# Performance work log

Measured on AMD Instinct MI355X. Metric: run time of the kernel, lower is better.

## Reference

```python
import jax, jax.numpy as jnp
import numpy as np


def setup_inputs() -> dict:
    key = jax.random.key(0)
    k1, k2, k3 = jax.random.split(key, 3)
    B, C_IN, C_OUT, K, S = 2, 16, 16, 3, 24
    x = jax.random.normal(k1, (B, C_IN, S, S, S, S), dtype=jnp.float32)
    # weight in canonical [out, in, kh, kw, kd, kt] layout (the torch module's
    # pre-permutation is a storage detail; the math is a standard 4D cross-correlation)
    w = jax.random.normal(k2, (C_OUT, C_IN, K, K, K, K), dtype=jnp.float32) * 0.05
    b = jax.random.normal(k3, (C_OUT,), dtype=jnp.float32) * 0.05
    return {"x": x, "w": w, "b": b}


def reference(x, w, b):
    # 4D convolution with 'same' padding (pad = k//2 in every spatial dim),
    # stride 1, no dilation — exactly what the looped conv4d() computes.
    dn = jax.lax.conv_dimension_numbers(x.shape, w.shape, ("NCHWDT", "OIHWDT", "NCHWDT"))
    out = jax.lax.conv_general_dilated(
        x, w,
        window_strides=(1, 1, 1, 1),
        padding="SAME",
        dimension_numbers=dn,
    )
    return out + b[None, :, None, None, None, None]
```

## Files before the change

kernel.cpp:

```cpp
#include <hip/hip_runtime.h>

typedef __attribute__((ext_vector_type(8))) short bfrag;
typedef __attribute__((ext_vector_type(4))) float f32x4;

#define XS4 331776
#define XS3 13824
#define XS2 576

__global__ void wsplit_kernel(const float* __restrict__ w,
                              unsigned int* __restrict__ wfrag) {
    int e = blockIdx.x * 256 + threadIdx.x;
    int ci2 = e & 3;
    int co  = (e >> 2) & 15;
    int t84 = e >> 6;
    int tau = t84 % 84;
    int cs  = t84 / 84;
    int ch  = cs >> 1;
    int s   = cs & 1;

    unsigned int outv = 0u;
    if (tau < 81) {
        unsigned int half[2];
#pragma unroll
        for (int q = 0; q < 2; ++q) {
            int ci = ch * 8 + ci2 * 2 + q;
            union { float f; unsigned u; } v;
            v.f = w[(co * 16 + ci) * 81 + tau];
            unsigned hi = v.u & 0xFFFF0000u;
            union { unsigned u; float f; } hv; hv.u = hi;
            union { float f; unsigned u; } rv; rv.f = v.f - hv.f;
            unsigned lo = rv.u & 0xFFFF0000u;
            half[q] = (s == 0) ? hi : lo;
        }
        outv = (half[0] >> 16) | (half[1] & 0xFFFF0000u);
    }
    wfrag[e] = outv;
}

__global__ __launch_bounds__(192, 3)
void conv4d_mfma(const float* __restrict__ x,
                 const unsigned short* __restrict__ wfrag,
                 const float* __restrict__ bias,
                 float* __restrict__ out) {
    __shared__ __align__(16) unsigned short xhl[2][1260][8];

    const int tid = threadIdx.x;
    const int l   = tid & 63;

    int bid = blockIdx.x;
    const int b    = bid / 3456;
    int r          = bid % 3456;
    const int h    = r / 144;
    r              = r % 144;
    const int w0   = r / 6;
    const int seg  = r % 6;
    const int dseg = seg >> 1;
    const int tseg = seg & 1;
    const int dbase = dseg * 8, tbase = tseg * 12;

    const int i_  = l & 15;
    const int tl4 = l >> 4;
    const int d_i = i_ >> 2;
    const int t_i = i_ & 3;
    const int co  = l & 15;

    const int wv  = tid >> 6;
    const int mt0 = wv * 2, mt1 = wv * 2 + 1;
    const int dq0 = mt0 / 3, tq0 = mt0 % 3;
    const int dq1 = mt1 / 3, tq1 = mt1 % 3;
    const int la0 = dq0 * 896 + tq0 * 64 + d_i * 224 + t_i * 16;
    const int la1 = dq1 * 896 + tq1 * 64 + d_i * 224 + t_i * 16;

    f32x4 acc0 = {0.f, 0.f, 0.f, 0.f};
    f32x4 acc1 = {0.f, 0.f, 0.f, 0.f};

    const char* xbase = (const char*)&xhl[0][0][0];
    const char* wB    = (const char*)wfrag + tl4 * 256 + co * 16;

    for (int ch = 0; ch < 2; ++ch) {
        __syncthreads();

        for (int k = 0; k < 7; ++k) {
            int idx = tid + k * 192;
            if (idx < 1260) {
                int p  = idx / 140;
                int rr = idx - p * 140;
                int dd = rr / 14;
                int tt = rr - dd * 14;
                int hh = h  + p / 3 - 1;
                int ww = w0 + p % 3 - 1;
                int dp = dbase + dd - 1;
                int tp = tbase + tt - 1;
                unsigned hib[8], lob[8];
                bool valid = ((unsigned)hh < 24u) && ((unsigned)ww < 24u) &&
                             ((unsigned)dp < 24u) && ((unsigned)tp < 24u);
                if (valid) {
                    int g = b * (16 * XS4) + (ch * 8) * XS4
                          + hh * XS3 + ww * XS2 + dp * 24 + tp;
#pragma unroll
                    for (int c = 0; c < 8; ++c) {
                        union { float f; unsigned u; } v;
                        v.f = x[g + c * XS4];
                        unsigned hi = v.u & 0xFFFF0000u;
                        union { unsigned u; float f; } hv; hv.u = hi;
                        union { float f; unsigned u; } rv2; rv2.f = v.f - hv.f;
                        hib[c] = hi;
                        lob[c] = rv2.u & 0xFFFF0000u;
                    }
                } else {
#pragma unroll
                    for (int c = 0; c < 8; ++c) { hib[c] = 0u; lob[c] = 0u; }
                }
                uint4 ph, pl;
                ph.x = (hib[0] >> 16) | (hib[1] & 0xFFFF0000u);
                ph.y = (hib[2] >> 16) | (hib[3] & 0xFFFF0000u);
                ph.z = (hib[4] >> 16) | (hib[5] & 0xFFFF0000u);
                ph.w = (hib[6] >> 16) | (hib[7] & 0xFFFF0000u);
                pl.x = (lob[0] >> 16) | (lob[1] & 0xFFFF0000u);
                pl.y = (lob[2] >> 16) | (lob[3] & 0xFFFF0000u);
                pl.z = (lob[4] >> 16) | (lob[5] & 0xFFFF0000u);
                pl.w = (lob[6] >> 16) | (lob[7] & 0xFFFF0000u);
                *(uint4*)((char*)&xhl[0][0][0] + idx * 16)         = ph;
                *(uint4*)((char*)&xhl[0][0][0] + 20160 + idx * 16) = pl;
            }
        }
        __syncthreads();

        const char* pw = wB + ch * 43008;

#pragma unroll
        for (int g = 0; g < 21; ++g) {
            bfrag whf = *(const bfrag*)(pw + g * 1024);
            bfrag wlf = *(const bfrag*)(pw + g * 1024 + 21504);

            int tau  = 4 * g + tl4;
            int teff = tau > 80 ? 80 : tau;
            int p    = teff / 9;
            int r9   = teff - p * 9;
            int kd   = r9 / 3;
            int kt   = r9 - kd * 3;
            int aoff = p * 2240 + kd * 224 + kt * 16;

            const char* ax = xbase + aoff;
            bfrag xh0 = *(const bfrag*)(ax + la0);
            bfrag xl0 = *(const bfrag*)(ax + la0 + 20160);
            bfrag xh1 = *(const bfrag*)(ax + la1);
            bfrag xl1 = *(const bfrag*)(ax + la1 + 20160);

            acc0 = __builtin_amdgcn_mfma_f32_16x16x32_bf16(xh0, whf, acc0, 0, 0, 0);
            acc1 = __builtin_amdgcn_mfma_f32_16x16x32_bf16(xh1, whf, acc1, 0, 0, 0);
            acc0 = __builtin_amdgcn_mfma_f32_16x16x32_bf16(xh0, wlf, acc0, 0, 0, 0);
            acc1 = __builtin_amdgcn_mfma_f32_16x16x32_bf16(xh1, wlf, acc1, 0, 0, 0);
            acc0 = __builtin_amdgcn_mfma_f32_16x16x32_bf16(xl0, whf, acc0, 0, 0, 0);
            acc1 = __builtin_amdgcn_mfma_f32_16x16x32_bf16(xl1, whf, acc1, 0, 0, 0);
        }
    }

    const float bv = bias[co];
    const int ob = (b * 16 + co) * XS4 + h * XS3 + w0 * XS2;
    {
        int d = dbase + dq0 * 4 + tl4;
        int t = tbase + tq0 * 4;
        float4 v;
        v.x = acc0[0] + bv; v.y = acc0[1] + bv;
        v.z = acc0[2] + bv; v.w = acc0[3] + bv;
        *(float4*)&out[ob + d * 24 + t] = v;
    }
    {
        int d = dbase + dq1 * 4 + tl4;
        int t = tbase + tq1 * 4;
        float4 v;
        v.x = acc1[0] + bv; v.y = acc1[1] + bv;
        v.z = acc1[2] + bv; v.w = acc1[3] + bv;
        *(float4*)&out[ob + d * 24 + t] = v;
    }
}

extern "C" void kernel_launch(void* const* d_in, const int* in_sizes, int n_in,
                              void* d_out, int out_size, void* d_ws, size_t ws_size,
                              hipStream_t stream) {
    const float* x    = (const float*)d_in[0];
    const float* w    = (const float*)d_in[1];
    const float* bias = (const float*)d_in[2];
    float* out        = (float*)d_out;
    unsigned int* wsw = (unsigned int*)d_ws;

    wsplit_kernel<<<84, 256, 0, stream>>>(w, wsw);
    conv4d_mfma<<<6912, 192, 0, stream>>>(x, (const unsigned short*)wsw, bias, out);
}
```

Baseline: 243.1 us.

## Pre-split input to bf16 hi/lo in workspace and stage via global_load_lds

Adds a separate pass that splits the fp32 input once into packed bf16 hi/lo halves in workspace. The conv kernel then copies 16-byte records straight into LDS with global_load_lds, using a zero buffer for padded sites. This removes the redundant per-block split of halo data, which covers about 9x the tile, and the strided 8-channel gathers. In exchange it costs an extra full read and write of the input, needs a large workspace with a fallback path, and adds setprio around the MFMA groups plus precomputed LDS offsets.

```diff
diff --git a/kernel.cpp b/kernel.cpp
--- a/kernel.cpp
+++ b/kernel.cpp
@@ -7,8 +7,16 @@
 #define XS3 13824
 #define XS2 576
 
+#define WS_ZERO   86016
+#define WS_XS     86080
+#define XS_HALF_B 5308416
+#define WS_NEED   42553408ull
+#define NSITE     1260
+#define NSITE_PAD 1280
+#define LDS_LO    20480
+
 __global__ void wsplit_kernel(const float* __restrict__ w,
-                              unsigned int* __restrict__ wfrag) {
+                              unsigned int* __restrict__ ws) {
     int e = blockIdx.x * 256 + threadIdx.x;
     int ci2 = e & 3;
     int co  = (e >> 2) & 15;
@@ -34,18 +42,50 @@
         }
         outv = (half[0] >> 16) | (half[1] & 0xFFFF0000u);
     }
-    wfrag[e] = outv;
+    ws[e] = outv;
+    if (e < 16) ws[(WS_ZERO / 4) + e] = 0u;
+}
+
+__global__ void xsplit_kernel(const float* __restrict__ x,
+                              unsigned short* __restrict__ xs) {
+    int s4 = blockIdx.x * 256 + threadIdx.x;
+    int bc = blockIdx.y;
+    const float* xp = x + (size_t)(bc * 8) * XS4 + s4;
+    unsigned hib[8], lob[8];
+#pragma unroll
+    for (int c = 0; c < 8; ++c) {
+        union { float f; unsigned u; } v;
+        v.f = xp[(size_t)c * XS4];
+        unsigned hi = v.u & 0xFFFF0000u;
+        union { unsigned u; float f; } hv; hv.u = hi;
+        union { float f; unsigned u; } rv; rv.f = v.f - hv.f;
+        hib[c] = hi;
+        lob[c] = rv.u & 0xFFFF0000u;
+    }
+    uint4 ph, pl;
+    ph.x = (hib[0] >> 16) | (hib[1] & 0xFFFF0000u);
+    ph.y = (hib[2] >> 16) | (hib[3] & 0xFFFF0000u);
+    ph.z = (hib[4] >> 16) | (hib[5] & 0xFFFF0000u);
+    ph.w = (hib[6] >> 16) | (hib[7] & 0xFFFF0000u);
+    pl.x = (lob[0] >> 16) | (lob[1] & 0xFFFF0000u);
+    pl.y = (lob[2] >> 16) | (lob[3] & 0xFFFF0000u);
+    pl.z = (lob[4] >> 16) | (lob[5] & 0xFFFF0000u);
+    pl.w = (lob[6] >> 16) | (lob[7] & 0xFFFF0000u);
+    *(uint4*)(xs + ((size_t)(bc * 2 + 0) * XS4 + s4) * 8) = ph;
+    *(uint4*)(xs + ((size_t)(bc * 2 + 1) * XS4 + s4) * 8) = pl;
 }
 
 __global__ __launch_bounds__(192, 3)
-void conv4d_mfma(const float* __restrict__ x,
-                 const unsigned short* __restrict__ wfrag,
-                 const float* __restrict__ bias,
-                 float* __restrict__ out) {
-    __shared__ __align__(16) unsigned short xhl[2][1260][8];
-
-    const int tid = threadIdx.x;
-    const int l   = tid & 63;
+void conv4d_mfma_v2(const unsigned short* __restrict__ xs,
+                    const unsigned short* __restrict__ wfrag,
+                    const char* __restrict__ zptr,
+                    const float* __restrict__ bias,
+                    float* __restrict__ out) {
+    __shared__ __align__(16) unsigned short xhl[2 * NSITE_PAD * 8];
+
+    const int tid  = threadIdx.x;
+    const int l    = tid & 63;
+    const int wv   = tid >> 6;
 
     int bid = blockIdx.x;
     const int b    = bid / 3456;
@@ -54,9 +94,140 @@
     r              = r % 144;
     const int w0   = r / 6;
     const int seg  = r % 6;
-    const int dseg = seg >> 1;
-    const int tseg = seg & 1;
-    const int dbase = dseg * 8, tbase = tseg * 12;
+    const int dbase = (seg >> 1) * 8, tbase = (seg & 1) * 12;
+
+    const int i_  = l & 15;
+    const int tl4 = l >> 4;
+    const int d_i = i_ >> 2;
+    const int t_i = i_ & 3;
+    const int co  = l & 15;
+
+    const int mt0 = wv * 2, mt1 = wv * 2 + 1;
+    const int dq0 = mt0 / 3, tq0 = mt0 % 3;
+    const int dq1 = mt1 / 3, tq1 = mt1 % 3;
+    const int la0 = dq0 * 896 + tq0 * 64 + d_i * 224 + t_i * 16;
+    const int la1 = dq1 * 896 + tq1 * 64 + d_i * 224 + t_i * 16;
+
+    int aoffs[21];
+#pragma unroll
+    for (int g = 0; g < 21; ++g) {
+        int tau  = 4 * g + tl4;
+        int teff = tau > 80 ? 80 : tau;
+        int p    = teff / 9;
+        int r9   = teff - p * 9;
+        int kd   = r9 / 3;
+        int kt   = r9 - kd * 3;
+        aoffs[g] = p * 2240 + kd * 224 + kt * 16;
+    }
+
+    f32x4 acc0 = {0.f, 0.f, 0.f, 0.f};
+    f32x4 acc1 = {0.f, 0.f, 0.f, 0.f};
+
+    const char* xbase = (const char*)&xhl[0];
+    const char* xsb   = (const char*)xs;
+    const char* wB    = (const char*)wfrag + tl4 * 256 + co * 16;
+
+    for (int ch = 0; ch < 2; ++ch) {
+        __syncthreads();
+
+        const unsigned base16 = (unsigned)((b * 2 + ch) * 2) * (unsigned)(XS4 * 16);
+
+        for (int k = 0; k < 7; ++k) {
+            int idx0 = k * 192 + wv * 64;
+            if (idx0 < NSITE_PAD) {
+                int idx = idx0 + l;
+                int p  = idx / 140;
+                int rr = idx - p * 140;
+                int dd = rr / 14;
+                int tt = rr - dd * 14;
+                int hh = h  + p / 3 - 1;
+                int ww = w0 + p % 3 - 1;
+                int dp = dbase + dd - 1;
+                int tp = tbase + tt - 1;
+                bool valid = ((unsigned)hh < 24u) && ((unsigned)ww < 24u) &&
+                             ((unsigned)dp < 24u) && ((unsigned)tp < 24u) &&
+                             (idx < NSITE);
+                const char* gh = zptr;
+                const char* gl = zptr;
+                if (valid) {
+                    unsigned off = base16 +
+                        (unsigned)(hh * XS3 + ww * XS2 + dp * 24 + tp) * 16u;
+                    gh = xsb + off;
+                    gl = gh + XS_HALF_B;
+                }
+                char* lp = (char*)&xhl[0] + idx * 16;
+                __builtin_amdgcn_global_load_lds(
+                    (const __attribute__((address_space(1))) void*)gh,
+                    (__attribute__((address_space(3))) void*)lp, 16, 0, 0);
+                __builtin_amdgcn_global_load_lds(
+                    (const __attribute__((address_space(1))) void*)gl,
+                    (__attribute__((address_space(3))) void*)(lp + LDS_LO), 16, 0, 0);
+            }
+        }
+        __syncthreads();
+
+        const char* pw = wB + ch * 43008;
+
+#pragma unroll
+        for (int g = 0; g < 21; ++g) {
+            bfrag whf = *(const bfrag*)(pw + g * 1024);
+            bfrag wlf = *(const bfrag*)(pw + g * 1024 + 21504);
+
+            const char* ax = xbase + aoffs[g];
+            bfrag xh0 = *(const bfrag*)(ax + la0);
+            bfrag xl0 = *(const bfrag*)(ax + la0 + LDS_LO);
+            bfrag xh1 = *(const bfrag*)(ax + la1);
+            bfrag xl1 = *(const bfrag*)(ax + la1 + LDS_LO);
+
+            __builtin_amdgcn_s_setprio(1);
+            acc0 = __builtin_amdgcn_mfma_f32_16x16x32_bf16(xh0, whf, acc0, 0, 0, 0);
+            acc1 = __builtin_amdgcn_mfma_f32_16x16x32_bf16(xh1, whf, acc1, 0, 0, 0);
+            acc0 = __builtin_amdgcn_mfma_f32_16x16x32_bf16(xh0, wlf, acc0, 0, 0, 0);
+            acc1 = __builtin_amdgcn_mfma_f32_16x16x32_bf16(xh1, wlf, acc1, 0, 0, 0);
+            acc0 = __builtin_amdgcn_mfma_f32_16x16x32_bf16(xl0, whf, acc0, 0, 0, 0);
+            acc1 = __builtin_amdgcn_mfma_f32_16x16x32_bf16(xl1, whf, acc1, 0, 0, 0);
+            __builtin_amdgcn_s_setprio(0);
+        }
+    }
+
+    const float bv = bias[co];
+    const int ob = (b * 16 + co) * XS4 + h * XS3 + w0 * XS2;
+    {
+        int d = dbase + dq0 * 4 + tl4;
+        int t = tbase + tq0 * 4;
+        float4 v;
+        v.x = acc0[0] + bv; v.y = acc0[1] + bv;
+        v.z = acc0[2] + bv; v.w = acc0[3] + bv;
+        *(float4*)&out[ob + d * 24 + t] = v;
+    }
+    {
+        int d = dbase + dq1 * 4 + tl4;
+        int t = tbase + tq1 * 4;
+        float4 v;
+        v.x = acc1[0] + bv; v.y = acc1[1] + bv;
+        v.z = acc1[2] + bv; v.w = acc1[3] + bv;
+        *(float4*)&out[ob + d * 24 + t] = v;
+    }
+}
+
+__global__ __launch_bounds__(192, 3)
+void conv4d_mfma_v1(const float* __restrict__ x,
+                    const unsigned short* __restrict__ wfrag,
+                    const float* __restrict__ bias,
+                    float* __restrict__ out) {
+    __shared__ __align__(16) unsigned short xhl[2][1260][8];
+
+    const int tid = threadIdx.x;
+    const int l   = tid & 63;
+
+    int bid = blockIdx.x;
+    const int b    = bid / 3456;
+    int r          = bid % 3456;
+    const int h    = r / 144;
+    r              = r % 144;
+    const int w0   = r / 6;
+    const int seg  = r % 6;
+    const int dbase = (seg >> 1) * 8, tbase = (seg & 1) * 12;
 
     const int i_  = l & 15;
     const int tl4 = l >> 4;
@@ -79,7 +250,6 @@
 
     for (int ch = 0; ch < 2; ++ch) {
         __syncthreads();
-
         for (int k = 0; k < 7; ++k) {
             int idx = tid + k * 192;
             if (idx < 1260) {
@@ -127,7 +297,6 @@
         __syncthreads();
 
         const char* pw = wB + ch * 43008;
-
 #pragma unroll
         for (int g = 0; g < 21; ++g) {
             bfrag whf = *(const bfrag*)(pw + g * 1024);
@@ -183,8 +352,18 @@
     const float* w    = (const float*)d_in[1];
     const float* bias = (const float*)d_in[2];
     float* out        = (float*)d_out;
-    unsigned int* wsw = (unsigned int*)d_ws;
-
-    wsplit_kernel<<<84, 256, 0, stream>>>(w, wsw);
-    conv4d_mfma<<<6912, 192, 0, stream>>>(x, (const unsigned short*)wsw, bias, out);
-}
+    char* ws          = (char*)d_ws;
+    unsigned* wfrag   = (unsigned*)ws;
+
+    wsplit_kernel<<<84, 256, 0, stream>>>(w, wfrag);
+
+    if (ws_size >= WS_NEED) {
+        unsigned short* xs = (unsigned short*)(ws + WS_XS);
+        xsplit_kernel<<<dim3(1296, 4), 256, 0, stream>>>(x, xs);
+        conv4d_mfma_v2<<<6912, 192, 0, stream>>>(
+            xs, (const unsigned short*)wfrag, ws + WS_ZERO, bias, out);
+    } else {
+        conv4d_mfma_v1<<<6912, 192, 0, stream>>>(
+            x, (const unsigned short*)wfrag, bias, out);
+    }
+}
```

Measured after the change: 231.2 us. 1.05x faster.
